# Kernel optimization log

Hardware: AMD Instinct MI355X
Metric: run time of the kernel (lower is better)

Reference implementation:

```python
import jax, jax.numpy as jnp
import numpy as np

N_NODES = 20000
N_EDGES = 640000
IN_DIM, HIDDEN, OUT_DIM = 128, 256, 64
EPS = 1e-12


def setup_inputs() -> dict:
    key = jax.random.key(0)
    ks = jax.random.split(key, 8)
    x = jax.random.normal(ks[0], (N_NODES, IN_DIM), dtype=jnp.float32)
    edge_src = jax.random.randint(ks[1], (N_EDGES,), 0, N_NODES, dtype=jnp.int32)
    edge_dst = jax.random.randint(ks[2], (N_EDGES,), 0, N_NODES, dtype=jnp.int32)
    s1 = 1.0 / np.sqrt(IN_DIM)
    s2 = 1.0 / np.sqrt(HIDDEN)
    W1 = jax.random.uniform(ks[3], (IN_DIM, HIDDEN), jnp.float32, -s1, s1)
    b1 = jax.random.uniform(ks[4], (HIDDEN,), jnp.float32, -s1, s1)
    W2 = jax.random.uniform(ks[5], (HIDDEN, OUT_DIM), jnp.float32, -s2, s2)
    b2 = jax.random.uniform(ks[6], (OUT_DIM,), jnp.float32, -s2, s2)
    return {"x": x, "edge_src": edge_src, "edge_dst": edge_dst,
            "W1": W1, "b1": b1, "W2": W2, "b2": b2}


def _agnn_layer(h, src, dst, n_nodes):
    # AGNN propagation with beta = 1 (non-trainable buffer in source module):
    # out_i = sum_j softmax_j(cos(h_i, h_j)) * h_j over neighbors j (incl. self-loop)
    hn = h * jax.lax.rsqrt(jnp.sum(h * h, axis=-1, keepdims=True) + EPS)
    logits = jnp.sum(hn[src] * hn[dst], axis=-1)            # [E] cosine similarity
    m = jax.ops.segment_max(logits, dst, num_segments=n_nodes)
    e = jnp.exp(logits - m[dst])
    z = jax.ops.segment_sum(e, dst, num_segments=n_nodes)
    alpha = e / z[dst]                                       # per-dst softmax
    return jax.ops.segment_sum(alpha[:, None] * h[src], dst, num_segments=n_nodes)


def reference(x, edge_src, edge_dst, W1, b1, W2, b2):
    n = x.shape[0]
    loop = jnp.arange(n, dtype=edge_src.dtype)
    src = jnp.concatenate([edge_src, loop])
    dst = jnp.concatenate([edge_dst, loop])
    h = jax.nn.relu(x @ W1 + b1)
    for _ in range(4):
        h = jax.nn.relu(_agnn_layer(h, src, dst, n))
    return h @ W2 + b2
```

## Files before the change

kernel.cpp:

```cpp
#include <hip/hip_runtime.h>

#define N_NODES 20000
#define N_EDGES 640000
#define E_TOT   (N_EDGES + N_NODES)
#define IN_DIM  128
#define HIDDEN  256
#define OUT_DIM 64
#define LOG2E 1.4426950408889634f

typedef __attribute__((ext_vector_type(2))) float f32x2;

__device__ __forceinline__ unsigned short f2bf(float f) {
    union { float f; unsigned int i; } x; x.f = f;
    unsigned int u = x.i;
    return (unsigned short)((u + 0x7fffu + ((u >> 16) & 1u)) >> 16);
}
__device__ __forceinline__ f32x2 up2(unsigned int p) {
    f32x2 r;
    r.x = __uint_as_float(p << 16);
    r.y = __uint_as_float(p & 0xffff0000u);
    return r;
}
__device__ __forceinline__ unsigned int pk2(float a, float b) {
    return (unsigned int)f2bf(a) | ((unsigned int)f2bf(b) << 16);
}


__global__ void zero_cnt_kernel(int* __restrict__ cnt) {
    int i = blockIdx.x * blockDim.x + threadIdx.x;
    if (i < N_NODES) cnt[i] = 0;
}

__global__ void count_kernel(const int* __restrict__ edge_dst, int* __restrict__ cnt) {
    int i = blockIdx.x * blockDim.x + threadIdx.x;
    if (i >= E_TOT) return;
    int d = (i < N_EDGES) ? edge_dst[i] : (i - N_EDGES);
    atomicAdd(&cnt[d], 1);
}

__global__ __launch_bounds__(1024) void scan_kernel(int* __restrict__ cnt, int* __restrict__ indptr) {
    const int T = 1024;
    const int C = (N_NODES + T - 1) / T;
    __shared__ int sums[T];
    int t = threadIdx.x;
    int base = t * C;
    int local[C];
    int s = 0;
#pragma unroll
    for (int i = 0; i < C; i++) {
        int idx = base + i;
        int v = (idx < N_NODES) ? cnt[idx] : 0;
        local[i] = s;
        s += v;
    }
    sums[t] = s;
    __syncthreads();
    for (int off = 1; off < T; off <<= 1) {
        int v = (t >= off) ? sums[t - off] : 0;
        __syncthreads();
        sums[t] += v;
        __syncthreads();
    }
    int prefix = (t == 0) ? 0 : sums[t - 1];
#pragma unroll
    for (int i = 0; i < C; i++) {
        int idx = base + i;
        if (idx < N_NODES) {
            indptr[idx] = prefix + local[i];
            cnt[idx] = 0;
        }
    }
    if (t == T - 1) indptr[N_NODES] = prefix + s;
}

__global__ void scatter_kernel(const int* __restrict__ edge_src, const int* __restrict__ edge_dst,
                               const int* __restrict__ indptr, int* __restrict__ cnt,
                               int* __restrict__ ssrc) {
    int i = blockIdx.x * blockDim.x + threadIdx.x;
    if (i >= E_TOT) return;
    int d, s;
    if (i < N_EDGES) { d = edge_dst[i]; s = edge_src[i]; }
    else             { d = i - N_EDGES; s = d; }
    int pos = indptr[d] + atomicAdd(&cnt[d], 1);
    ssrc[pos] = s;
}


__global__ __launch_bounds__(256) void gemm_bias_act(const float* __restrict__ A,
                                                     const float* __restrict__ B,
                                                     const float* __restrict__ bias,
                                                     float* __restrict__ C,
                                                     int M, int Nn, int K, int relu) {
    __shared__ float As[16][65];
    __shared__ float Bs[16][65];
    int tid = threadIdx.x;
    int tx = tid & 15, ty = tid >> 4;
    int row0 = blockIdx.x * 64, col0 = blockIdx.y * 64;
    float acc[4][4] = {};
    for (int k0 = 0; k0 < K; k0 += 16) {
        {
            int r_ = tid >> 2;
            int kq = (tid & 3) * 4;
            int gr = row0 + r_;
            float4 a4 = make_float4(0.f, 0.f, 0.f, 0.f);
            if (gr < M) a4 = *(const float4*)&A[(long)gr * K + k0 + kq];
            As[kq + 0][r_] = a4.x; As[kq + 1][r_] = a4.y;
            As[kq + 2][r_] = a4.z; As[kq + 3][r_] = a4.w;
        }
        {
            int kr = tid >> 4;
            int cq = (tid & 15) * 4;
            float4 b4 = *(const float4*)&B[(long)(k0 + kr) * Nn + col0 + cq];
            Bs[kr][cq + 0] = b4.x; Bs[kr][cq + 1] = b4.y;
            Bs[kr][cq + 2] = b4.z; Bs[kr][cq + 3] = b4.w;
        }
        __syncthreads();
#pragma unroll
        for (int kk = 0; kk < 16; kk++) {
            float a[4], b[4];
#pragma unroll
            for (int i = 0; i < 4; i++) a[i] = As[kk][ty * 4 + i];
#pragma unroll
            for (int j = 0; j < 4; j++) b[j] = Bs[kk][tx * 4 + j];
#pragma unroll
            for (int i = 0; i < 4; i++)
#pragma unroll
                for (int j = 0; j < 4; j++) acc[i][j] += a[i] * b[j];
        }
        __syncthreads();
    }
#pragma unroll
    for (int i = 0; i < 4; i++) {
        int gr = row0 + ty * 4 + i;
        if (gr >= M) continue;
#pragma unroll
        for (int j = 0; j < 4; j++) {
            int gc = col0 + tx * 4 + j;
            float v = acc[i][j] + bias[gc];
            if (relu) v = fmaxf(v, 0.f);
            C[(long)gr * Nn + gc] = v;
        }
    }
}


__global__ __launch_bounds__(256) void normalize0_kernel(const float* __restrict__ h,
                                                         unsigned short* __restrict__ hnb,
                                                         float* __restrict__ r) {
    int i = blockIdx.x;
    int c = threadIdx.x;
    float v = h[(long)i * HIDDEN + c];
    float ss = v * v;
#pragma unroll
    for (int off = 32; off; off >>= 1) ss += __shfl_xor(ss, off);
    __shared__ float wsum[4];
    int wid = c >> 6, lane = c & 63;
    if (lane == 0) wsum[wid] = ss;
    __syncthreads();
    float tot = wsum[0] + wsum[1] + wsum[2] + wsum[3];
    float rr = sqrtf(tot + 1e-12f);
    hnb[(long)i * HIDDEN + c] = f2bf(v / rr);
    if (c == 0) r[i] = rr;
}


__global__ __launch_bounds__(256) void agnn_kernel(const unsigned short* __restrict__ hnb,
                                                   const float* __restrict__ rin,
                                                   const int* __restrict__ indptr,
                                                   const int* __restrict__ ssrc,
                                                   unsigned short* __restrict__ hnout,
                                                   float* __restrict__ rout,
                                                   float* __restrict__ hout,
                                                   int write_hn) {
    int lane = threadIdx.x & 63;
    int wid  = threadIdx.x >> 6;
    int gid  = lane >> 4;
    int gl   = lane & 15;
    int node = blockIdx.x * 16 + wid * 4 + gid;

    const uint4* tab4 = (const uint4*)hnb;
    long nb = (long)node * 32 + gl * 2;
    uint4 ha = tab4[nb], hb = tab4[nb + 1];
    f32x2 hd2[8];
    {
        f32x2 t;
        t = up2(ha.x); hd2[0] = t * LOG2E;
        t = up2(ha.y); hd2[1] = t * LOG2E;
        t = up2(ha.z); hd2[2] = t * LOG2E;
        t = up2(ha.w); hd2[3] = t * LOG2E;
        t = up2(hb.x); hd2[4] = t * LOG2E;
        t = up2(hb.y); hd2[5] = t * LOG2E;
        t = up2(hb.z); hd2[6] = t * LOG2E;
        t = up2(hb.w); hd2[7] = t * LOG2E;
    }

    int beg = indptr[node], end = indptr[node + 1];
    int n = end - beg;
    int last = end - 1;

    f32x2 acc[8];
#pragma unroll
    for (int p = 0; p < 8; p++) acc[p] = (f32x2)0.f;
    float z = 0.f;

    int s = ssrc[beg];
    long sb = (long)s * 32 + gl * 2;
    uint4 va = tab4[sb], vb = tab4[sb + 1];
    float rs = rin[s];

    for (int i = 0; i < n; i++) {
        uint4 ca = va, cb = vb;
        float cr = rs;
        {
            int nx = beg + i + 1;
            nx = (nx > last) ? last : nx;
            int s2 = ssrc[nx];
            long b2 = (long)s2 * 32 + gl * 2;
            va = tab4[b2]; vb = tab4[b2 + 1];
            rs = rin[s2];
        }
        f32x2 cf[8];
        cf[0] = up2(ca.x); cf[1] = up2(ca.y); cf[2] = up2(ca.z); cf[3] = up2(ca.w);
        cf[4] = up2(cb.x); cf[5] = up2(cb.y); cf[6] = up2(cb.z); cf[7] = up2(cb.w);
        f32x2 d2a = cf[0] * hd2[0];
        f32x2 d2b = cf[1] * hd2[1];
        d2a += cf[2] * hd2[2];  d2b += cf[3] * hd2[3];
        d2a += cf[4] * hd2[4];  d2b += cf[5] * hd2[5];
        d2a += cf[6] * hd2[6];  d2b += cf[7] * hd2[7];
        f32x2 d2 = d2a + d2b;
        float d = d2.x + d2.y;
        d += __shfl_xor(d, 1, 16);
        d += __shfl_xor(d, 2, 16);
        d += __shfl_xor(d, 4, 16);
        d += __shfl_xor(d, 8, 16);
        float w = exp2f(d);
        z += w;
        float wr = w * cr;
#pragma unroll
        for (int p = 0; p < 8; p++) acc[p] += cf[p] * wr;
    }

    float inv = 1.f / z;
    f32x2 o[8];
#pragma unroll
    for (int p = 0; p < 8; p++) {
        f32x2 t = acc[p] * inv;
        t.x = fmaxf(t.x, 0.f);
        t.y = fmaxf(t.y, 0.f);
        o[p] = t;
    }

    if (write_hn) {
        float ss = 0.f;
#pragma unroll
        for (int p = 0; p < 8; p++) ss += o[p].x * o[p].x + o[p].y * o[p].y;
        ss += __shfl_xor(ss, 1, 16);
        ss += __shfl_xor(ss, 2, 16);
        ss += __shfl_xor(ss, 4, 16);
        ss += __shfl_xor(ss, 8, 16);
        float rr = sqrtf(ss + 1e-12f);
        float ir = 1.f / rr;
        uint4 oa, ob;
        oa.x = pk2(o[0].x * ir, o[0].y * ir);
        oa.y = pk2(o[1].x * ir, o[1].y * ir);
        oa.z = pk2(o[2].x * ir, o[2].y * ir);
        oa.w = pk2(o[3].x * ir, o[3].y * ir);
        ob.x = pk2(o[4].x * ir, o[4].y * ir);
        ob.y = pk2(o[5].x * ir, o[5].y * ir);
        ob.z = pk2(o[6].x * ir, o[6].y * ir);
        ob.w = pk2(o[7].x * ir, o[7].y * ir);
        uint4* outt = (uint4*)hnout;
        outt[nb] = oa;
        outt[nb + 1] = ob;
        if (gl == 0) rout[node] = rr;
    } else {
        float4* ho = (float4*)(hout + (long)node * HIDDEN + gl * 16);
        ho[0] = make_float4(o[0].x, o[0].y, o[1].x, o[1].y);
        ho[1] = make_float4(o[2].x, o[2].y, o[3].x, o[3].y);
        ho[2] = make_float4(o[4].x, o[4].y, o[5].x, o[5].y);
        ho[3] = make_float4(o[6].x, o[6].y, o[7].x, o[7].y);
    }
}


extern "C" void kernel_launch(void* const* d_in, const int* in_sizes, int n_in,
                              void* d_out, int out_size, void* d_ws, size_t ws_size,
                              hipStream_t stream) {
    const float* x  = (const float*)d_in[0];
    const int* esrc = (const int*)d_in[1];
    const int* edst = (const int*)d_in[2];
    const float* W1 = (const float*)d_in[3];
    const float* b1 = (const float*)d_in[4];
    const float* W2 = (const float*)d_in[5];
    const float* b2 = (const float*)d_in[6];
    float* out = (float*)d_out;

    char* ws = (char*)d_ws;
    float*          h0     = (float*)(ws);
    unsigned short* hnA    = (unsigned short*)(ws + 20480000);
    unsigned short* hnB    = (unsigned short*)(ws + 30720000);
    float*          rA     = (float*)(ws + 40960000);
    float*          rB     = (float*)(ws + 41040000);
    int*            indptr = (int*)  (ws + 41120000);
    int*            cnt    = (int*)  (ws + 41200256);
    int*            ssrc   = (int*)  (ws + 41280256);

    zero_cnt_kernel<<<(N_NODES + 255) / 256, 256, 0, stream>>>(cnt);
    count_kernel<<<(E_TOT + 255) / 256, 256, 0, stream>>>(edst, cnt);
    scan_kernel<<<1, 1024, 0, stream>>>(cnt, indptr);
    scatter_kernel<<<(E_TOT + 255) / 256, 256, 0, stream>>>(esrc, edst, indptr, cnt, ssrc);

    dim3 g1((N_NODES + 63) / 64, HIDDEN / 64);
    gemm_bias_act<<<g1, 256, 0, stream>>>(x, W1, b1, h0, N_NODES, HIDDEN, IN_DIM, 1);

    normalize0_kernel<<<N_NODES, 256, 0, stream>>>(h0, hnA, rA);

    int nblk = N_NODES / 16;
    agnn_kernel<<<nblk, 256, 0, stream>>>(hnA, rA, indptr, ssrc, hnB, rB, h0, 1);
    agnn_kernel<<<nblk, 256, 0, stream>>>(hnB, rB, indptr, ssrc, hnA, rA, h0, 1);
    agnn_kernel<<<nblk, 256, 0, stream>>>(hnA, rA, indptr, ssrc, hnB, rB, h0, 1);
    agnn_kernel<<<nblk, 256, 0, stream>>>(hnB, rB, indptr, ssrc, hnA, rA, h0, 0);

    dim3 g2((N_NODES + 63) / 64, OUT_DIM / 64);
    gemm_bias_act<<<g2, 256, 0, stream>>>(h0, W2, b2, out, N_NODES, OUT_DIM, HIDDEN, 0);
}
```

Before: 349.2 us.

## Use 32 lanes per node and deepen neighbor prefetch in AGNN kernel

Each node in the AGNN aggregation is now handled by 32 lanes instead of 16, so each lane loads one 16-byte chunk of the bf16 row rather than two. The grid doubles to match. The neighbor prefetch goes from one edge ahead to two, and the two nodes sharing a wavefront loop to the larger degree of the pair, with masked weights past the end. This aims at more memory-level parallelism and fewer registers per lane for the gather-bound loop. The cost is an extra shuffle step per edge and idle iterations when the two paired nodes have different degrees.

```diff
diff --git a/kernel.cpp b/kernel.cpp
--- a/kernel.cpp
+++ b/kernel.cpp
@@ -172,78 +172,74 @@
                                                    float* __restrict__ rout,
                                                    float* __restrict__ hout,
                                                    int write_hn) {
-    int lane = threadIdx.x & 63;
-    int wid  = threadIdx.x >> 6;
-    int gid  = lane >> 4;
-    int gl   = lane & 15;
-    int node = blockIdx.x * 16 + wid * 4 + gid;
+    int wid = threadIdx.x >> 6;
+    int g   = (threadIdx.x >> 5) & 1;
+    int gl  = threadIdx.x & 31;
+    int node = blockIdx.x * 8 + wid * 2 + g;
 
     const uint4* tab4 = (const uint4*)hnb;
-    long nb = (long)node * 32 + gl * 2;
-    uint4 ha = tab4[nb], hb = tab4[nb + 1];
-    f32x2 hd2[8];
-    {
-        f32x2 t;
-        t = up2(ha.x); hd2[0] = t * LOG2E;
-        t = up2(ha.y); hd2[1] = t * LOG2E;
-        t = up2(ha.z); hd2[2] = t * LOG2E;
-        t = up2(ha.w); hd2[3] = t * LOG2E;
-        t = up2(hb.x); hd2[4] = t * LOG2E;
-        t = up2(hb.y); hd2[5] = t * LOG2E;
-        t = up2(hb.z); hd2[6] = t * LOG2E;
-        t = up2(hb.w); hd2[7] = t * LOG2E;
-    }
+    long nb = (long)node * 32 + gl;
+    uint4 hv = tab4[nb];
+    f32x2 hd2[4];
+    hd2[0] = up2(hv.x) * LOG2E;
+    hd2[1] = up2(hv.y) * LOG2E;
+    hd2[2] = up2(hv.z) * LOG2E;
+    hd2[3] = up2(hv.w) * LOG2E;
 
     int beg = indptr[node], end = indptr[node + 1];
     int n = end - beg;
     int last = end - 1;
-
-    f32x2 acc[8];
-#pragma unroll
-    for (int p = 0; p < 8; p++) acc[p] = (f32x2)0.f;
+    int nmax = max(n, __shfl_xor(n, 32));
+
+    f32x2 acc[4];
+#pragma unroll
+    for (int p = 0; p < 4; p++) acc[p] = (f32x2)0.f;
     float z = 0.f;
 
-    int s = ssrc[beg];
-    long sb = (long)s * 32 + gl * 2;
-    uint4 va = tab4[sb], vb = tab4[sb + 1];
-    float rs = rin[s];
-
-    for (int i = 0; i < n; i++) {
-        uint4 ca = va, cb = vb;
-        float cr = rs;
-        {
-            int nx = beg + i + 1;
-            nx = (nx > last) ? last : nx;
-            int s2 = ssrc[nx];
-            long b2 = (long)s2 * 32 + gl * 2;
-            va = tab4[b2]; vb = tab4[b2 + 1];
-            rs = rin[s2];
-        }
-        f32x2 cf[8];
-        cf[0] = up2(ca.x); cf[1] = up2(ca.y); cf[2] = up2(ca.z); cf[3] = up2(ca.w);
-        cf[4] = up2(cb.x); cf[5] = up2(cb.y); cf[6] = up2(cb.z); cf[7] = up2(cb.w);
+    int e1 = (1 > last - beg) ? last : beg + 1;
+    int e2 = (2 > last - beg) ? last : beg + 2;
+    int s0 = ssrc[beg];
+    int s1 = ssrc[e1];
+    uint4 v0 = tab4[(long)s0 * 32 + gl];
+    float r0 = rin[s0];
+    uint4 v1 = tab4[(long)s1 * 32 + gl];
+    float r1 = rin[s1];
+    int s2 = ssrc[e2];
+
+    for (int i = 0; i < nmax; i++) {
+        uint4 cv = v0;
+        float cr = r0;
+        v0 = v1; r0 = r1;
+        v1 = tab4[(long)s2 * 32 + gl];
+        r1 = rin[s2];
+        int e3 = beg + i + 3;
+        e3 = (e3 > last) ? last : e3;
+        s2 = ssrc[e3];
+
+        f32x2 cf[4];
+        cf[0] = up2(cv.x); cf[1] = up2(cv.y); cf[2] = up2(cv.z); cf[3] = up2(cv.w);
         f32x2 d2a = cf[0] * hd2[0];
         f32x2 d2b = cf[1] * hd2[1];
-        d2a += cf[2] * hd2[2];  d2b += cf[3] * hd2[3];
-        d2a += cf[4] * hd2[4];  d2b += cf[5] * hd2[5];
-        d2a += cf[6] * hd2[6];  d2b += cf[7] * hd2[7];
+        d2a += cf[2] * hd2[2];
+        d2b += cf[3] * hd2[3];
         f32x2 d2 = d2a + d2b;
         float d = d2.x + d2.y;
-        d += __shfl_xor(d, 1, 16);
-        d += __shfl_xor(d, 2, 16);
-        d += __shfl_xor(d, 4, 16);
-        d += __shfl_xor(d, 8, 16);
-        float w = exp2f(d);
+        d += __shfl_xor(d, 1);
+        d += __shfl_xor(d, 2);
+        d += __shfl_xor(d, 4);
+        d += __shfl_xor(d, 8);
+        d += __shfl_xor(d, 16);
+        float w = (i < n) ? exp2f(d) : 0.f;
         z += w;
         float wr = w * cr;
 #pragma unroll
-        for (int p = 0; p < 8; p++) acc[p] += cf[p] * wr;
+        for (int p = 0; p < 4; p++) acc[p] += cf[p] * wr;
     }
 
     float inv = 1.f / z;
-    f32x2 o[8];
-#pragma unroll
-    for (int p = 0; p < 8; p++) {
+    f32x2 o[4];
+#pragma unroll
+    for (int p = 0; p < 4; p++) {
         f32x2 t = acc[p] * inv;
         t.x = fmaxf(t.x, 0.f);
         t.y = fmaxf(t.y, 0.f);
@@ -253,32 +249,25 @@
     if (write_hn) {
         float ss = 0.f;
 #pragma unroll
-        for (int p = 0; p < 8; p++) ss += o[p].x * o[p].x + o[p].y * o[p].y;
-        ss += __shfl_xor(ss, 1, 16);
-        ss += __shfl_xor(ss, 2, 16);
-        ss += __shfl_xor(ss, 4, 16);
-        ss += __shfl_xor(ss, 8, 16);
+        for (int p = 0; p < 4; p++) ss += o[p].x * o[p].x + o[p].y * o[p].y;
+        ss += __shfl_xor(ss, 1);
+        ss += __shfl_xor(ss, 2);
+        ss += __shfl_xor(ss, 4);
+        ss += __shfl_xor(ss, 8);
+        ss += __shfl_xor(ss, 16);
         float rr = sqrtf(ss + 1e-12f);
         float ir = 1.f / rr;
-        uint4 oa, ob;
-        oa.x = pk2(o[0].x * ir, o[0].y * ir);
-        oa.y = pk2(o[1].x * ir, o[1].y * ir);
-        oa.z = pk2(o[2].x * ir, o[2].y * ir);
-        oa.w = pk2(o[3].x * ir, o[3].y * ir);
-        ob.x = pk2(o[4].x * ir, o[4].y * ir);
-        ob.y = pk2(o[5].x * ir, o[5].y * ir);
-        ob.z = pk2(o[6].x * ir, o[6].y * ir);
-        ob.w = pk2(o[7].x * ir, o[7].y * ir);
-        uint4* outt = (uint4*)hnout;
-        outt[nb] = oa;
-        outt[nb + 1] = ob;
+        uint4 ov;
+        ov.x = pk2(o[0].x * ir, o[0].y * ir);
+        ov.y = pk2(o[1].x * ir, o[1].y * ir);
+        ov.z = pk2(o[2].x * ir, o[2].y * ir);
+        ov.w = pk2(o[3].x * ir, o[3].y * ir);
+        ((uint4*)hnout)[nb] = ov;
         if (gl == 0) rout[node] = rr;
     } else {
-        float4* ho = (float4*)(hout + (long)node * HIDDEN + gl * 16);
+        float4* ho = (float4*)(hout + (long)node * HIDDEN + gl * 8);
         ho[0] = make_float4(o[0].x, o[0].y, o[1].x, o[1].y);
         ho[1] = make_float4(o[2].x, o[2].y, o[3].x, o[3].y);
-        ho[2] = make_float4(o[4].x, o[4].y, o[5].x, o[5].y);
-        ho[3] = make_float4(o[6].x, o[6].y, o[7].x, o[7].y);
     }
 }
 
@@ -315,7 +304,7 @@
 
     normalize0_kernel<<<N_NODES, 256, 0, stream>>>(h0, hnA, rA);
 
-    int nblk = N_NODES / 16;
+    int nblk = N_NODES / 8;
     agnn_kernel<<<nblk, 256, 0, stream>>>(hnA, rA, indptr, ssrc, hnB, rB, h0, 1);
     agnn_kernel<<<nblk, 256, 0, stream>>>(hnB, rB, indptr, ssrc, hnA, rA, h0, 1);
     agnn_kernel<<<nblk, 256, 0, stream>>>(hnA, rA, indptr, ssrc, hnB, rB, h0, 1);
```

Result: slower. 390.3 us (+11.7%).

## Degree-sort nodes and split each node's edges across two 16-lane groups

Applied to the files above, without the earlier changes.

Adds a counting sort of nodes by in-degree, descending, to build a permutation, so each wavefront handles nodes of similar degree and divergence from uneven edge counts shrinks. Each node now gets two 16-lane groups that each process half of its edge list, with a two-deep prefetch pipeline, and their partial sums are combined with cross-lane shuffles. The GEMM also switches to float4 shared-memory reads and writes with padding of 68. The cost is four extra small preprocessing kernels, redundant epilogue work in the second group, and scattered output writes.

```diff
diff --git a/kernel.cpp b/kernel.cpp
--- a/kernel.cpp
+++ b/kernel.cpp
@@ -7,6 +7,7 @@
 #define HIDDEN  256
 #define OUT_DIM 64
 #define LOG2E 1.4426950408889634f
+#define NBIN 1024
 
 typedef __attribute__((ext_vector_type(2))) float f32x2;
 
@@ -86,13 +87,54 @@
 }
 
 
+__global__ void hist_zero_kernel(int* __restrict__ hist, int* __restrict__ hcur) {
+    int i = blockIdx.x * blockDim.x + threadIdx.x;
+    if (i < NBIN) { hist[i] = 0; hcur[i] = 0; }
+}
+
+__global__ void deg_hist_kernel(const int* __restrict__ indptr, int* __restrict__ hist) {
+    int i = blockIdx.x * blockDim.x + threadIdx.x;
+    if (i >= N_NODES) return;
+    int d = indptr[i + 1] - indptr[i];
+    int k = (d > NBIN - 1) ? (NBIN - 1) : d;
+    atomicAdd(&hist[NBIN - 1 - k], 1);
+}
+
+__global__ __launch_bounds__(NBIN) void hist_scan_kernel(const int* __restrict__ hist,
+                                                         int* __restrict__ hbase) {
+    __shared__ int sm[NBIN];
+    int t = threadIdx.x;
+    int v = hist[t];
+    sm[t] = v;
+    __syncthreads();
+    for (int off = 1; off < NBIN; off <<= 1) {
+        int u = (t >= off) ? sm[t - off] : 0;
+        __syncthreads();
+        sm[t] += u;
+        __syncthreads();
+    }
+    hbase[t] = sm[t] - v;
+}
+
+__global__ void perm_scatter_kernel(const int* __restrict__ indptr, const int* __restrict__ hbase,
+                                    int* __restrict__ hcur, int* __restrict__ perm) {
+    int i = blockIdx.x * blockDim.x + threadIdx.x;
+    if (i >= N_NODES) return;
+    int d = indptr[i + 1] - indptr[i];
+    int k = (d > NBIN - 1) ? (NBIN - 1) : d;
+    int key = NBIN - 1 - k;
+    int pos = hbase[key] + atomicAdd(&hcur[key], 1);
+    perm[pos] = i;
+}
+
+
 __global__ __launch_bounds__(256) void gemm_bias_act(const float* __restrict__ A,
                                                      const float* __restrict__ B,
                                                      const float* __restrict__ bias,
                                                      float* __restrict__ C,
                                                      int M, int Nn, int K, int relu) {
-    __shared__ float As[16][65];
-    __shared__ float Bs[16][65];
+    __shared__ float As[16][68];
+    __shared__ float Bs[16][68];
     int tid = threadIdx.x;
     int tx = tid & 15, ty = tid >> 4;
     int row0 = blockIdx.x * 64, col0 = blockIdx.y * 64;
@@ -111,17 +153,15 @@
             int kr = tid >> 4;
             int cq = (tid & 15) * 4;
             float4 b4 = *(const float4*)&B[(long)(k0 + kr) * Nn + col0 + cq];
-            Bs[kr][cq + 0] = b4.x; Bs[kr][cq + 1] = b4.y;
-            Bs[kr][cq + 2] = b4.z; Bs[kr][cq + 3] = b4.w;
+            *(float4*)&Bs[kr][cq] = b4;
         }
         __syncthreads();
 #pragma unroll
         for (int kk = 0; kk < 16; kk++) {
-            float a[4], b[4];
-#pragma unroll
-            for (int i = 0; i < 4; i++) a[i] = As[kk][ty * 4 + i];
-#pragma unroll
-            for (int j = 0; j < 4; j++) b[j] = Bs[kk][tx * 4 + j];
+            float4 a4 = *(const float4*)&As[kk][ty * 4];
+            float4 b4 = *(const float4*)&Bs[kk][tx * 4];
+            float a[4] = {a4.x, a4.y, a4.z, a4.w};
+            float b[4] = {b4.x, b4.y, b4.z, b4.w};
 #pragma unroll
             for (int i = 0; i < 4; i++)
 #pragma unroll
@@ -168,76 +208,86 @@
                                                    const float* __restrict__ rin,
                                                    const int* __restrict__ indptr,
                                                    const int* __restrict__ ssrc,
+                                                   const int* __restrict__ perm,
                                                    unsigned short* __restrict__ hnout,
                                                    float* __restrict__ rout,
                                                    float* __restrict__ hout,
                                                    int write_hn) {
     int lane = threadIdx.x & 63;
     int wid  = threadIdx.x >> 6;
-    int gid  = lane >> 4;
+    int half = lane >> 5;
+    int sub  = (lane >> 4) & 1;
     int gl   = lane & 15;
-    int node = blockIdx.x * 16 + wid * 4 + gid;
+    int node = perm[blockIdx.x * 8 + wid * 2 + half];
 
     const uint4* tab4 = (const uint4*)hnb;
     long nb = (long)node * 32 + gl * 2;
     uint4 ha = tab4[nb], hb = tab4[nb + 1];
     f32x2 hd2[8];
-    {
-        f32x2 t;
-        t = up2(ha.x); hd2[0] = t * LOG2E;
-        t = up2(ha.y); hd2[1] = t * LOG2E;
-        t = up2(ha.z); hd2[2] = t * LOG2E;
-        t = up2(ha.w); hd2[3] = t * LOG2E;
-        t = up2(hb.x); hd2[4] = t * LOG2E;
-        t = up2(hb.y); hd2[5] = t * LOG2E;
-        t = up2(hb.z); hd2[6] = t * LOG2E;
-        t = up2(hb.w); hd2[7] = t * LOG2E;
-    }
+    hd2[0] = up2(ha.x) * LOG2E; hd2[1] = up2(ha.y) * LOG2E;
+    hd2[2] = up2(ha.z) * LOG2E; hd2[3] = up2(ha.w) * LOG2E;
+    hd2[4] = up2(hb.x) * LOG2E; hd2[5] = up2(hb.y) * LOG2E;
+    hd2[6] = up2(hb.z) * LOG2E; hd2[7] = up2(hb.w) * LOG2E;
 
     int beg = indptr[node], end = indptr[node + 1];
-    int n = end - beg;
-    int last = end - 1;
+    int deg = end - beg;
+    int c0  = (deg + 1) >> 1;
+    int cnt = sub ? (deg - c0) : c0;
+    int eb  = beg + (sub ? c0 : 0);
+    int lim = (cnt > 0) ? (eb + cnt - 1) : beg;
+    int nmax = max(cnt, __shfl_xor(cnt, 16));
+    nmax = max(nmax, __shfl_xor(nmax, 32));
 
     f32x2 acc[8];
 #pragma unroll
     for (int p = 0; p < 8; p++) acc[p] = (f32x2)0.f;
     float z = 0.f;
 
-    int s = ssrc[beg];
-    long sb = (long)s * 32 + gl * 2;
-    uint4 va = tab4[sb], vb = tab4[sb + 1];
-    float rs = rin[s];
-
-    for (int i = 0; i < n; i++) {
-        uint4 ca = va, cb = vb;
-        float cr = rs;
-        {
-            int nx = beg + i + 1;
-            nx = (nx > last) ? last : nx;
-            int s2 = ssrc[nx];
-            long b2 = (long)s2 * 32 + gl * 2;
-            va = tab4[b2]; vb = tab4[b2 + 1];
-            rs = rin[s2];
-        }
+    int s0 = ssrc[(0 < cnt) ? eb : lim];
+    int s1 = ssrc[min(eb + 1, lim)];
+    long b0 = (long)s0 * 32 + gl * 2;
+    uint4 v0a = tab4[b0], v0b = tab4[b0 + 1];
+    float r0 = rin[s0];
+    long b1 = (long)s1 * 32 + gl * 2;
+    uint4 v1a = tab4[b1], v1b = tab4[b1 + 1];
+    float r1 = rin[s1];
+    int s2 = ssrc[min(eb + 2, lim)];
+
+    for (int i = 0; i < nmax; i++) {
+        uint4 ca = v0a, cb = v0b;
+        float cr = r0;
+        v0a = v1a; v0b = v1b; r0 = r1;
+        long b2 = (long)s2 * 32 + gl * 2;
+        v1a = tab4[b2]; v1b = tab4[b2 + 1];
+        r1 = rin[s2];
+        s2 = ssrc[min(eb + i + 3, lim)];
+
         f32x2 cf[8];
         cf[0] = up2(ca.x); cf[1] = up2(ca.y); cf[2] = up2(ca.z); cf[3] = up2(ca.w);
         cf[4] = up2(cb.x); cf[5] = up2(cb.y); cf[6] = up2(cb.z); cf[7] = up2(cb.w);
-        f32x2 d2a = cf[0] * hd2[0];
-        f32x2 d2b = cf[1] * hd2[1];
-        d2a += cf[2] * hd2[2];  d2b += cf[3] * hd2[3];
-        d2a += cf[4] * hd2[4];  d2b += cf[5] * hd2[5];
-        d2a += cf[6] * hd2[6];  d2b += cf[7] * hd2[7];
-        f32x2 d2 = d2a + d2b;
+        f32x2 da = cf[0] * hd2[0];
+        f32x2 db = cf[1] * hd2[1];
+        da += cf[2] * hd2[2];  db += cf[3] * hd2[3];
+        da += cf[4] * hd2[4];  db += cf[5] * hd2[5];
+        da += cf[6] * hd2[6];  db += cf[7] * hd2[7];
+        f32x2 d2 = da + db;
         float d = d2.x + d2.y;
-        d += __shfl_xor(d, 1, 16);
-        d += __shfl_xor(d, 2, 16);
-        d += __shfl_xor(d, 4, 16);
-        d += __shfl_xor(d, 8, 16);
-        float w = exp2f(d);
+        d += __shfl_xor(d, 1);
+        d += __shfl_xor(d, 2);
+        d += __shfl_xor(d, 4);
+        d += __shfl_xor(d, 8);
+        float w = (i < cnt) ? exp2f(d) : 0.f;
         z += w;
         float wr = w * cr;
 #pragma unroll
         for (int p = 0; p < 8; p++) acc[p] += cf[p] * wr;
+    }
+
+    z += __shfl_xor(z, 16);
+#pragma unroll
+    for (int p = 0; p < 8; p++) {
+        acc[p].x += __shfl_xor(acc[p].x, 16);
+        acc[p].y += __shfl_xor(acc[p].y, 16);
     }
 
     float inv = 1.f / z;
@@ -254,31 +304,35 @@
         float ss = 0.f;
 #pragma unroll
         for (int p = 0; p < 8; p++) ss += o[p].x * o[p].x + o[p].y * o[p].y;
-        ss += __shfl_xor(ss, 1, 16);
-        ss += __shfl_xor(ss, 2, 16);
-        ss += __shfl_xor(ss, 4, 16);
-        ss += __shfl_xor(ss, 8, 16);
+        ss += __shfl_xor(ss, 1);
+        ss += __shfl_xor(ss, 2);
+        ss += __shfl_xor(ss, 4);
+        ss += __shfl_xor(ss, 8);
         float rr = sqrtf(ss + 1e-12f);
         float ir = 1.f / rr;
-        uint4 oa, ob;
-        oa.x = pk2(o[0].x * ir, o[0].y * ir);
-        oa.y = pk2(o[1].x * ir, o[1].y * ir);
-        oa.z = pk2(o[2].x * ir, o[2].y * ir);
-        oa.w = pk2(o[3].x * ir, o[3].y * ir);
-        ob.x = pk2(o[4].x * ir, o[4].y * ir);
-        ob.y = pk2(o[5].x * ir, o[5].y * ir);
-        ob.z = pk2(o[6].x * ir, o[6].y * ir);
-        ob.w = pk2(o[7].x * ir, o[7].y * ir);
-        uint4* outt = (uint4*)hnout;
-        outt[nb] = oa;
-        outt[nb + 1] = ob;
-        if (gl == 0) rout[node] = rr;
+        if (sub == 0) {
+            uint4 oa, ob;
+            oa.x = pk2(o[0].x * ir, o[0].y * ir);
+            oa.y = pk2(o[1].x * ir, o[1].y * ir);
+            oa.z = pk2(o[2].x * ir, o[2].y * ir);
+            oa.w = pk2(o[3].x * ir, o[3].y * ir);
+            ob.x = pk2(o[4].x * ir, o[4].y * ir);
+            ob.y = pk2(o[5].x * ir, o[5].y * ir);
+            ob.z = pk2(o[6].x * ir, o[6].y * ir);
+            ob.w = pk2(o[7].x * ir, o[7].y * ir);
+            uint4* outt = (uint4*)hnout;
+            outt[nb] = oa;
+            outt[nb + 1] = ob;
+            if (gl == 0) rout[node] = rr;
+        }
     } else {
-        float4* ho = (float4*)(hout + (long)node * HIDDEN + gl * 16);
-        ho[0] = make_float4(o[0].x, o[0].y, o[1].x, o[1].y);
-        ho[1] = make_float4(o[2].x, o[2].y, o[3].x, o[3].y);
-        ho[2] = make_float4(o[4].x, o[4].y, o[5].x, o[5].y);
-        ho[3] = make_float4(o[6].x, o[6].y, o[7].x, o[7].y);
+        if (sub == 0) {
+            float4* ho = (float4*)(hout + (long)node * HIDDEN + gl * 16);
+            ho[0] = make_float4(o[0].x, o[0].y, o[1].x, o[1].y);
+            ho[1] = make_float4(o[2].x, o[2].y, o[3].x, o[3].y);
+            ho[2] = make_float4(o[4].x, o[4].y, o[5].x, o[5].y);
+            ho[3] = make_float4(o[6].x, o[6].y, o[7].x, o[7].y);
+        }
     }
 }
 
@@ -304,22 +358,31 @@
     int*            indptr = (int*)  (ws + 41120000);
     int*            cnt    = (int*)  (ws + 41200256);
     int*            ssrc   = (int*)  (ws + 41280256);
+    int*            perm   = (int*)  (ws + 43920256);
+    int*            hist   = (int*)  (ws + 44000256);
+    int*            hbase  = (int*)  (ws + 44004352);
+    int*            hcur   = (int*)  (ws + 44008448);
 
     zero_cnt_kernel<<<(N_NODES + 255) / 256, 256, 0, stream>>>(cnt);
     count_kernel<<<(E_TOT + 255) / 256, 256, 0, stream>>>(edst, cnt);
     scan_kernel<<<1, 1024, 0, stream>>>(cnt, indptr);
     scatter_kernel<<<(E_TOT + 255) / 256, 256, 0, stream>>>(esrc, edst, indptr, cnt, ssrc);
 
+    hist_zero_kernel<<<(NBIN + 255) / 256, 256, 0, stream>>>(hist, hcur);
+    deg_hist_kernel<<<(N_NODES + 255) / 256, 256, 0, stream>>>(indptr, hist);
+    hist_scan_kernel<<<1, NBIN, 0, stream>>>(hist, hbase);
+    perm_scatter_kernel<<<(N_NODES + 255) / 256, 256, 0, stream>>>(indptr, hbase, hcur, perm);
+
     dim3 g1((N_NODES + 63) / 64, HIDDEN / 64);
     gemm_bias_act<<<g1, 256, 0, stream>>>(x, W1, b1, h0, N_NODES, HIDDEN, IN_DIM, 1);
 
     normalize0_kernel<<<N_NODES, 256, 0, stream>>>(h0, hnA, rA);
 
-    int nblk = N_NODES / 16;
-    agnn_kernel<<<nblk, 256, 0, stream>>>(hnA, rA, indptr, ssrc, hnB, rB, h0, 1);
-    agnn_kernel<<<nblk, 256, 0, stream>>>(hnB, rB, indptr, ssrc, hnA, rA, h0, 1);
-    agnn_kernel<<<nblk, 256, 0, stream>>>(hnA, rA, indptr, ssrc, hnB, rB, h0, 1);
-    agnn_kernel<<<nblk, 256, 0, stream>>>(hnB, rB, indptr, ssrc, hnA, rA, h0, 0);
+    int nblk = N_NODES / 8;
+    agnn_kernel<<<nblk, 256, 0, stream>>>(hnA, rA, indptr, ssrc, perm, hnB, rB, h0, 1);
+    agnn_kernel<<<nblk, 256, 0, stream>>>(hnB, rB, indptr, ssrc, perm, hnA, rA, h0, 1);
+    agnn_kernel<<<nblk, 256, 0, stream>>>(hnA, rA, indptr, ssrc, perm, hnB, rB, h0, 1);
+    agnn_kernel<<<nblk, 256, 0, stream>>>(hnB, rB, indptr, ssrc, perm, hnA, rA, h0, 0);
 
     dim3 g2((N_NODES + 63) / 64, OUT_DIM / 64);
     gemm_bias_act<<<g2, 256, 0, stream>>>(h0, W2, b2, out, N_NODES, OUT_DIM, HIDDEN, 0);
```

Result: slower. 397.2 us (+13.7%).
